# Kernel tuning notes

Measured on AMD Instinct MI355X. Metric: run time of the kernel, lower is better.

## Reference

```python
import jax, jax.numpy as jnp
import numpy as np

D = 2048      # hidden_size
S = 2048      # seq_len (batch packed, batch=1)
H = 16        # num_attention_heads
QL = 1536     # q_lora_rank
KVL = 512     # kv_lora_rank (latent dim, also v head size)
DN = 128      # qk_nope_head_dim
DR = 64       # qk_rope_head_dim
DV = 128      # v_head_dim
I = 8192      # mlp intermediate
EPS = 1e-6
SCALE = (DN + DR) ** -0.5  # softmax_scale = q_head_dim**-0.5 (no yarn mscale)


def rmsnorm(x, w):
    return x * jax.lax.rsqrt(jnp.mean(x * x, axis=-1, keepdims=True) + EPS) * w


def rotate_half(x):
    h = x.shape[-1] // 2
    return jnp.concatenate([-x[..., h:], x[..., :h]], axis=-1)


def setup_inputs() -> dict:
    key = jax.random.key(0)
    ks = jax.random.split(key, 10)
    s = 0.02
    # real RoPE tables (rotate_half layout)
    inv_freq = 1.0 / (10000.0 ** (jnp.arange(0, DR, 2, dtype=jnp.float32) / DR))
    t = jnp.arange(S, dtype=jnp.float32)
    emb = jnp.concatenate([jnp.outer(t, inv_freq)] * 2, axis=-1)  # [S, DR]
    return {
        'hidden_states': jax.random.normal(ks[0], (1, S, D), dtype=jnp.float32),
        'cos': jnp.cos(emb),
        'sin': jnp.sin(emb),
        'ln1_w': jnp.ones((D,), jnp.float32),
        'q_a_w': jax.random.normal(ks[1], (D, QL)) * s,
        'q_a_ln_w': jnp.ones((QL,), jnp.float32),
        'q_b_w': jax.random.normal(ks[2], (QL, H * (DN + DR))) * s,
        'kv_a_w': jax.random.normal(ks[3], (D, KVL + DR)) * s,
        'kv_a_ln_w': jnp.ones((KVL,), jnp.float32),
        'kc_w': jax.random.normal(ks[4], (H, DN, KVL)) * s,
        'vc_w': jax.random.normal(ks[5], (H, KVL, DV)) * s,
        'o_w': jax.random.normal(ks[6], (H * DV, D)) * s,
        'ln2_w': jnp.ones((D,), jnp.float32),
        'gate_up_w': jax.random.normal(ks[7], (D, 2 * I)) * s,
        'down_w': jax.random.normal(ks[8], (I, D)) * s,
    }


def reference(hidden_states, cos, sin, ln1_w, q_a_w, q_a_ln_w, q_b_w,
              kv_a_w, kv_a_ln_w, kc_w, vc_w, o_w, ln2_w, gate_up_w, down_w):
    residual = hidden_states
    h = rmsnorm(hidden_states, ln1_w)[0]                      # [S, D]
    # --- Q path: low-rank down + RMSNorm + up, split nope/rope ---
    q = rmsnorm(h @ q_a_w, q_a_ln_w) @ q_b_w                  # [S, H*(DN+DR)]
    q = q.reshape(S, H, DN + DR)
    q_nope, q_pe = q[..., :DN], q[..., DN:]
    # kc BMM: absorb W_UK, project q_nope into latent dim     # [S, H, KVL]
    q_lat = jnp.einsum('shd,hdc->shc', q_nope, kc_w)
    # --- KV path: compressed latent + shared rope key ---
    kv = h @ kv_a_w                                           # [S, KVL+DR]
    k_lat = rmsnorm(kv[:, :KVL], kv_a_ln_w)                   # [S, KVL] (also V)
    k_pe = kv[:, KVL:]                                        # [S, DR]
    # --- RoPE on the rope split only ---
    q_pe = q_pe * cos[:, None, :] + rotate_half(q_pe) * sin[:, None, :]
    k_pe = k_pe * cos + rotate_half(k_pe) * sin
    # --- latent MQA attention: q/k dim = KVL+DR, v dim = KVL ---
    qf = jnp.concatenate([q_lat, q_pe], axis=-1)              # [S, H, KVL+DR]
    kf = jnp.concatenate([k_lat, k_pe], axis=-1)              # [S, KVL+DR]
    scores = jnp.einsum('shc,tc->hst', qf, kf) * SCALE        # [H, S, S]
    causal = jnp.tril(jnp.ones((S, S), dtype=bool))
    scores = jnp.where(causal, scores, jnp.float32(-1e30))
    attn = jax.nn.softmax(scores, axis=-1)
    o_lat = jnp.einsum('hst,tc->shc', attn, k_lat)            # [S, H, KVL]
    # vc BMM: latent -> v_head_dim
    o = jnp.einsum('shc,hcv->shv', o_lat, vc_w).reshape(S, H * DV)
    attn_out = (o @ o_w)[None]                                # [1, S, D]
    hidden = residual + attn_out
    # --- dense SwiGLU MLP ---
    x2 = rmsnorm(hidden, ln2_w)
    gu = x2 @ gate_up_w
    mlp = (jax.nn.silu(gu[..., :I]) * gu[..., I:]) @ down_w
    return hidden + mlp
```

## Files before the change

kernel.cpp:

```cpp
#include <hip/hip_runtime.h>
#include <stdint.h>


#define S_   2048
#define D_   2048
#define H_   16
#define QL_  1536
#define KVL_ 512
#define DN_  128
#define DR_  64
#define DV_  128
#define I_   8192
#define SCALE_ 0.07216878364870323f

typedef __bf16 bf16x8 __attribute__((ext_vector_type(8)));
typedef float f32x4 __attribute__((ext_vector_type(4)));

__device__ __forceinline__ unsigned short f2bf(float f) {
  unsigned int u = __builtin_bit_cast(unsigned int, f);
  u += 0x7fffu + ((u >> 16) & 1u);
  return (unsigned short)(u >> 16);
}
__device__ __forceinline__ float bf2f(unsigned short b) {
  unsigned int u = ((unsigned int)b) << 16;
  return __builtin_bit_cast(float, u);
}

__device__ __forceinline__ float block_sum256(float v) {
  __shared__ float red[4];
  #pragma unroll
  for (int o = 32; o; o >>= 1) v += __shfl_xor(v, o);
  __syncthreads();
  if ((threadIdx.x & 63) == 0) red[threadIdx.x >> 6] = v;
  __syncthreads();
  return red[0] + red[1] + red[2] + red[3];
}
__device__ __forceinline__ float block_max256(float v) {
  __shared__ float red[4];
  #pragma unroll
  for (int o = 32; o; o >>= 1) v = fmaxf(v, __shfl_xor(v, o));
  __syncthreads();
  if ((threadIdx.x & 63) == 0) red[threadIdx.x >> 6] = v;
  __syncthreads();
  return fmaxf(fmaxf(red[0], red[1]), fmaxf(red[2], red[3]));
}

__device__ __forceinline__ void gload_lds16(const void* g, void* l) {
  void* gn = const_cast<void*>(g);
  __builtin_amdgcn_global_load_lds(
      (__attribute__((address_space(1))) void*)gn,
      (__attribute__((address_space(3))) void*)l, 16, 0, 0);
}

template <int OUT, int ADD_RES, int TRI, int CK>
__global__ __launch_bounds__(256) void gemm_bt(
    const unsigned short* __restrict__ A, const unsigned short* __restrict__ Bt,
    void* __restrict__ C, const float* __restrict__ R, float scale,
    int M, int N, int K, int lda, int ldb, int ldc,
    long sA, long sB, long sC) {
  __shared__ unsigned short As[128 * 64];
  __shared__ unsigned short Bs[128 * 64];
  const int b = blockIdx.z;
  int bx = blockIdx.x, by = blockIdx.y;
  if (TRI) {
    const int t = blockIdx.x;
    int i = (int)((sqrtf(8.f * t + 1.f) - 1.f) * 0.5f);
    while ((i + 1) * (i + 2) / 2 <= t) ++i;
    while (i * (i + 1) / 2 > t) --i;
    by = i;
    bx = t - i * (i + 1) / 2;
  }
  const int m0 = by * 128, n0 = bx * 128;
  if (CK) K = min(K, m0 + 128);
  const int tid = threadIdx.x, w = tid >> 6, lane = tid & 63;
  const int wm = (w >> 1) * 64, wn = (w & 1) * 64;
  const int fr = lane & 15;
  const int fq = lane >> 4;
  const int sr = lane >> 3;
  const int sch = (lane & 7) ^ sr;
  const unsigned short* Ab = A + (long)b * sA;
  const unsigned short* Bb = Bt + (long)b * sB;
  long aOff[4], bOff[4];
  #pragma unroll
  for (int i = 0; i < 4; ++i) {
    const int row = w * 32 + i * 8 + sr;
    aOff[i] = (long)(m0 + row) * lda + sch * 8;
    bOff[i] = (long)(n0 + row) * ldb + sch * 8;
  }
  const int ca0 = fq ^ (fr & 7);
  const int ca1 = (4 + fq) ^ (fr & 7);

  f32x4 acc[4][4] = {};

  for (int k0 = 0; k0 < K; k0 += 64) {
    #pragma unroll
    for (int i = 0; i < 4; ++i) {
      gload_lds16(Ab + aOff[i] + k0, As + (w * 32 + i * 8) * 64);
      gload_lds16(Bb + bOff[i] + k0, Bs + (w * 32 + i * 8) * 64);
    }
    __syncthreads();
    #pragma unroll
    for (int s = 0; s < 2; ++s) {
      const int cc = s ? ca1 : ca0;
      bf16x8 af[4], bf[4];
      #pragma unroll
      for (int i = 0; i < 4; ++i)
        af[i] = *(const bf16x8*)(As + (wm + i * 16 + fr) * 64 + cc * 8);
      #pragma unroll
      for (int j = 0; j < 4; ++j)
        bf[j] = *(const bf16x8*)(Bs + (wn + j * 16 + fr) * 64 + cc * 8);
      #pragma unroll
      for (int i = 0; i < 4; ++i)
        #pragma unroll
        for (int j = 0; j < 4; ++j)
          acc[i][j] = __builtin_amdgcn_mfma_f32_16x16x32_bf16(af[i], bf[j],
                                                              acc[i][j], 0, 0, 0);
    }
    __syncthreads();
  }

  const long cb = (long)b * sC;
  #pragma unroll
  for (int i = 0; i < 4; ++i) {
    const int row0 = m0 + wm + i * 16 + fq * 4;
    #pragma unroll
    for (int j = 0; j < 4; ++j) {
      const int col = n0 + wn + j * 16 + fr;
      #pragma unroll
      for (int r = 0; r < 4; ++r) {
        float v = acc[i][j][r] * scale;
        if (OUT == 2) {
          const float o = __shfl_xor(v, 1);
          const float res = v / (1.f + __expf(-v)) * o;
          if (((fr & 1) == 0) && col < N)
            ((unsigned short*)C)[cb + (long)(row0 + r) * ldc + (col >> 1)] =
                f2bf(res);
        } else {
          if (col < N) {
            const long idx = cb + (long)(row0 + r) * ldc + col;
            float vv = v;
            if (ADD_RES) vv += R[idx];
            if (OUT == 1) ((unsigned short*)C)[idx] = f2bf(vv);
            else          ((float*)C)[idx] = vv;
          }
        }
      }
    }
  }
}

__global__ void transpose_f2b(const float* __restrict__ in,
                              unsigned short* __restrict__ out, int Rr, int Cc,
                              long sIn, long sOut) {
  const int b = blockIdx.z;
  in += (long)b * sIn;
  out += (long)b * sOut;
  __shared__ float t[32][33];
  const int c0 = blockIdx.x * 32, r0 = blockIdx.y * 32;
  const int tx = threadIdx.x, ty = threadIdx.y;
  #pragma unroll
  for (int i = 0; i < 4; ++i)
    t[ty + i * 8][tx] = in[(long)(r0 + ty + i * 8) * Cc + c0 + tx];
  __syncthreads();
  #pragma unroll
  for (int i = 0; i < 4; ++i)
    out[(long)(c0 + ty + i * 8) * Rr + r0 + tx] = f2bf(t[tx][ty + i * 8]);
}

__global__ void transpose_f2b_ilv(const float* __restrict__ in,
                                  unsigned short* __restrict__ out) {
  __shared__ float t[32][33];
  const int c0 = blockIdx.x * 32, r0 = blockIdx.y * 32;
  const int tx = threadIdx.x, ty = threadIdx.y;
  #pragma unroll
  for (int i = 0; i < 4; ++i)
    t[ty + i * 8][tx] = in[(long)(r0 + ty + i * 8) * (2 * I_) + c0 + tx];
  __syncthreads();
  #pragma unroll
  for (int i = 0; i < 4; ++i) {
    const int c = c0 + ty + i * 8;
    const int n = ((c & (I_ - 1)) << 1) | (c >> 13);
    out[(long)n * D_ + r0 + tx] = f2bf(t[tx][ty + i * 8]);
  }
}

__global__ void rmsnorm_k(const float* __restrict__ x, const float* __restrict__ w,
                          unsigned short* __restrict__ y, int C) {
  const int row = blockIdx.x, tid = threadIdx.x;
  const float* xr = x + (long)row * C;
  float ss = 0.f;
  for (int c = tid; c < C; c += 256) { float v = xr[c]; ss += v * v; }
  ss = block_sum256(ss);
  const float rms = rsqrtf(ss / C + 1e-6f);
  for (int c = tid; c < C; c += 256)
    y[(long)row * C + c] = f2bf(xr[c] * rms * w[c]);
}

__global__ void q_post(const float* __restrict__ q, const float* __restrict__ cs,
                       const float* __restrict__ sn, unsigned short* __restrict__ qnope,
                       unsigned short* __restrict__ qf) {
  const int s = blockIdx.x, tid = threadIdx.x;
  const float* qr = q + (long)s * 3072;
  for (int c = tid; c < 3072; c += 256) {
    const int h = c / 192, d = c % 192;
    if (d < 128) {
      qnope[(long)s * 2048 + h * 128 + d] = f2bf(qr[c]);
    } else {
      const int j = d - 128;
      const float x = qr[c];
      const float rot = (j < 32) ? -qr[h * 192 + 128 + j + 32]
                                 :  qr[h * 192 + 128 + j - 32];
      const float v = x * cs[s * 64 + j] + rot * sn[s * 64 + j];
      qf[(long)h * (S_ * 576) + (long)s * 576 + 512 + j] = f2bf(v);
    }
  }
}

__global__ void kv_post(const float* __restrict__ kv, const float* __restrict__ w,
                        const float* __restrict__ cs, const float* __restrict__ sn,
                        unsigned short* __restrict__ kf, unsigned short* __restrict__ klt) {
  const int s = blockIdx.x, tid = threadIdx.x;
  const float* kr = kv + (long)s * 576;
  float ss = 0.f;
  for (int c = tid; c < 512; c += 256) { float v = kr[c]; ss += v * v; }
  ss = block_sum256(ss);
  const float rms = rsqrtf(ss / 512.f + 1e-6f);
  for (int c = tid; c < 576; c += 256) {
    if (c < 512) {
      const float v = kr[c] * rms * w[c];
      const unsigned short bv = f2bf(v);
      kf[(long)s * 576 + c] = bv;
      klt[(long)c * S_ + s] = bv;
    } else {
      const int j = c - 512;
      const float x = kr[c];
      const float rot = (j < 32) ? -kr[512 + j + 32] : kr[512 + j - 32];
      kf[(long)s * 576 + c] = f2bf(x * cs[s * 64 + j] + rot * sn[s * 64 + j]);
    }
  }
}

__global__ void softmax_causal_ip(unsigned short* __restrict__ sc, long hstride) {
  const int row = blockIdx.x, tid = threadIdx.x;
  unsigned short* sr = sc + (long)blockIdx.z * hstride + (long)row * S_;
  const int n = row + 1;
  const int kmax = ((row >> 7) + 1) << 7;
  float mx = -1e30f;
  for (int c = tid; c < n; c += 256) mx = fmaxf(mx, bf2f(sr[c]));
  mx = block_max256(mx);
  float e[8];
  float sum = 0.f;
  #pragma unroll
  for (int k = 0; k < 8; ++k) {
    const int c = tid + k * 256;
    if (c < n) { e[k] = __expf(bf2f(sr[c]) - mx); sum += e[k]; }
  }
  sum = block_sum256(sum);
  const float inv = 1.f / sum;
  #pragma unroll
  for (int k = 0; k < 8; ++k) {
    const int c = tid + k * 256;
    if (c < n) sr[c] = f2bf(e[k] * inv);
    else if (c < kmax) sr[c] = 0;
  }
}

extern "C" void kernel_launch(void* const* d_in, const int* in_sizes, int n_in,
                              void* d_out, int out_size, void* d_ws, size_t ws_size,
                              hipStream_t stream) {
  const float* hs   = (const float*)d_in[0];
  const float* cs   = (const float*)d_in[1];
  const float* sn   = (const float*)d_in[2];
  const float* ln1  = (const float*)d_in[3];
  const float* qaw  = (const float*)d_in[4];
  const float* qaln = (const float*)d_in[5];
  const float* qbw  = (const float*)d_in[6];
  const float* kvaw = (const float*)d_in[7];
  const float* kvln = (const float*)d_in[8];
  const float* kcw  = (const float*)d_in[9];
  const float* vcw  = (const float*)d_in[10];
  const float* ow   = (const float*)d_in[11];
  const float* ln2  = (const float*)d_in[12];
  const float* guw  = (const float*)d_in[13];
  const float* dww  = (const float*)d_in[14];
  float* out = (float*)d_out;
  char* ws = (char*)d_ws;

  unsigned short* hbf   = (unsigned short*)(ws + 0);
  float*          qa    = (float*)(ws + 8388608);
  unsigned short* qan   = (unsigned short*)(ws + 20971520);
  float*          q     = (float*)(ws + 27262976);
  unsigned short* qnope = (unsigned short*)(ws + 52428800);
  unsigned short* sc    = (unsigned short*)(ws + 0);
  unsigned short* qf    = (unsigned short*)(ws + 67108864);
  float*          kv    = (float*)(ws + 104857600);
  unsigned short* kf    = (unsigned short*)(ws + 109576192);
  unsigned short* klt   = (unsigned short*)(ws + 111935488);
  unsigned short* wt2   = (unsigned short*)(ws + 114032640);
  unsigned short* wt    = (unsigned short*)(ws + 116129792);
  unsigned short* olat  = (unsigned short*)(ws + 116129792);
  unsigned short* obf   = (unsigned short*)(ws + 0);
  float*          hidden= (float*)(ws + 8388608);
  unsigned short* x2    = (unsigned short*)(ws + 25165824);
  unsigned short* mlp   = (unsigned short*)(ws + 33554432);

  const dim3 B256(256), Bt32(32, 8);

  rmsnorm_k<<<S_, B256, 0, stream>>>(hs, ln1, hbf, D_);
  transpose_f2b<<<dim3(QL_/32, D_/32, 1), Bt32, 0, stream>>>(qaw, wt, D_, QL_, 0, 0);
  gemm_bt<0,0,0,0><<<dim3(QL_/128, S_/128, 1), B256, 0, stream>>>(
      hbf, wt, qa, nullptr, 1.f, S_, QL_, D_, D_, D_, QL_, 0, 0, 0);
  rmsnorm_k<<<S_, B256, 0, stream>>>(qa, qaln, qan, QL_);
  transpose_f2b<<<dim3(3072/32, QL_/32, 1), Bt32, 0, stream>>>(qbw, wt, QL_, 3072, 0, 0);
  gemm_bt<0,0,0,0><<<dim3(3072/128, S_/128, 1), B256, 0, stream>>>(
      qan, wt, q, nullptr, 1.f, S_, 3072, QL_, QL_, QL_, 3072, 0, 0, 0);
  q_post<<<S_, B256, 0, stream>>>(q, cs, sn, qnope, qf);
  transpose_f2b<<<dim3(576/32, D_/32, 1), Bt32, 0, stream>>>(kvaw, wt, D_, 576, 0, 0);
  gemm_bt<0,0,0,0><<<dim3(5, S_/128, 1), B256, 0, stream>>>(
      hbf, wt, kv, nullptr, 1.f, S_, 576, D_, D_, D_, 576, 0, 0, 0);
  kv_post<<<S_, B256, 0, stream>>>(kv, kvln, cs, sn, kf, klt);
  transpose_f2b<<<dim3(512/32, 128/32, H_), Bt32, 0, stream>>>(kcw, wt, 128, 512, 65536, 65536);
  transpose_f2b<<<dim3(128/32, 512/32, H_), Bt32, 0, stream>>>(vcw, wt2, 512, 128, 65536, 65536);
  gemm_bt<1,0,0,0><<<dim3(4, S_/128, H_), B256, 0, stream>>>(
      qnope, wt, qf, nullptr, 1.f, S_, 512, 128, 2048, 128, 576,
      128, 65536, (long)S_ * 576);
  for (int g = 0; g < 2; ++g) {
    const unsigned short* qfg = qf + (long)g * 8 * S_ * 576;
    gemm_bt<1,0,1,0><<<dim3(136, 1, 8), B256, 0, stream>>>(
        qfg, kf, sc, nullptr, SCALE_, S_, S_, 576, 576, 576, S_,
        (long)S_ * 576, 0, (long)S_ * S_);
    softmax_causal_ip<<<dim3(S_, 1, 8), B256, 0, stream>>>(sc, (long)S_ * S_);
    gemm_bt<1,0,0,1><<<dim3(4, 16, 8), B256, 0, stream>>>(
        sc, klt, olat + (long)g * 8 * S_ * 512, nullptr, 1.f,
        S_, 512, S_, S_, S_, 512, (long)S_ * S_, 0, (long)S_ * 512);
  }
  gemm_bt<1,0,0,0><<<dim3(1, S_/128, H_), B256, 0, stream>>>(
      olat, wt2, obf, nullptr, 1.f, S_, 128, 512, 512, 512, 2048,
      (long)S_ * 512, 65536, 128);
  transpose_f2b<<<dim3(D_/32, D_/32, 1), Bt32, 0, stream>>>(ow, wt, D_, D_, 0, 0);
  gemm_bt<0,1,0,0><<<dim3(D_/128, S_/128, 1), B256, 0, stream>>>(
      obf, wt, hidden, hs, 1.f, S_, D_, D_, D_, D_, D_, 0, 0, 0);
  rmsnorm_k<<<S_, B256, 0, stream>>>(hidden, ln2, x2, D_);
  transpose_f2b_ilv<<<dim3(2 * I_ / 32, D_/32, 1), Bt32, 0, stream>>>(guw, wt);
  gemm_bt<2,0,0,0><<<dim3(2 * I_ / 128, S_/128, 1), B256, 0, stream>>>(
      x2, wt, mlp, nullptr, 1.f, S_, 2 * I_, D_, D_, D_, I_, 0, 0, 0);
  transpose_f2b<<<dim3(D_/32, I_/32, 1), Bt32, 0, stream>>>(dww, wt, I_, D_, 0, 0);
  gemm_bt<0,1,0,0><<<dim3(D_/128, S_/128, 1), B256, 0, stream>>>(
      mlp, wt, out, hidden, 1.f, S_, D_, I_, I_, I_, D_, 0, 0, 0);
}
```

Baseline: 1.105 ms.

## Add 256x256 four-stage MFMA GEMM for scores and gate-up, widen transposes

Adds a new 512-thread GEMM kernel with 256x256 output tiles, a four-buffer LDS ring prefetching two K-steps ahead, XOR-swizzled LDS layout, an XCD-aware block remap, and split MFMA phases with priority hints. It is used for the causal QK^T score GEMM and the gate-up SwiGLU GEMM. The weight transpose kernels are replaced by a 64x64 tile version with float4 loads and 16-byte bf16 stores, with the interleave folded in as a template flag. The larger tiles aim to raise arithmetic intensity and cut global traffic, but use more registers and LDS, lowering occupancy. Edge handling for the 576-wide K and the triangular diagonal tiles rests on exact divisibility.

Result: no change. 1.119 ms (+1.2%).

```diff
diff --git a/kernel.cpp b/kernel.cpp
--- a/kernel.cpp
+++ b/kernel.cpp
@@ -15,6 +15,7 @@
 
 typedef __bf16 bf16x8 __attribute__((ext_vector_type(8)));
 typedef float f32x4 __attribute__((ext_vector_type(4)));
+typedef unsigned short us8 __attribute__((ext_vector_type(8)));
 
 __device__ __forceinline__ unsigned short f2bf(float f) {
   unsigned int u = __builtin_bit_cast(unsigned int, f);
@@ -50,6 +51,150 @@
   __builtin_amdgcn_global_load_lds(
       (__attribute__((address_space(1))) void*)gn,
       (__attribute__((address_space(3))) void*)l, 16, 0, 0);
+}
+
+template <int OUT, int TRI>
+__global__ __launch_bounds__(512, 2) void gemm256(
+    const unsigned short* __restrict__ A, const unsigned short* __restrict__ Bt,
+    void* __restrict__ C, float scale, int M, int N, int K,
+    int lda, int ldb, int ldc, long sA, long sB, long sC) {
+  __shared__ unsigned short As[4][8192];
+  __shared__ unsigned short Bs[4][8192];
+  const int b = blockIdx.z;
+  int bx = blockIdx.x, by = blockIdx.y;
+  if (TRI) {
+    const int t = blockIdx.x;
+    int i = (int)((sqrtf(8.f * t + 1.f) - 1.f) * 0.5f);
+    while ((i + 1) * (i + 2) / 2 <= t) ++i;
+    while (i * (i + 1) / 2 > t) --i;
+    by = i; bx = t - i * (i + 1) / 2;
+  } else {
+    int l = by * gridDim.x + bx;
+    const int nwg = gridDim.x * gridDim.y;
+    const int q = nwg >> 3, r = nwg & 7;
+    const int xcd = l & 7, pos = l >> 3;
+    l = (xcd < r ? xcd * (q + 1) : r * (q + 1) + (xcd - r) * q) + pos;
+    bx = l % gridDim.x; by = l / gridDim.x;
+  }
+  const int m0 = by * 256, n0 = bx * 256;
+  const int tid = threadIdx.x, w = tid >> 6, lane = tid & 63;
+  const int wm = w >> 2, wn = w & 3;
+  const int fr = lane & 15, fq = lane >> 4;
+  const unsigned short* Ab = A + (long)b * sA;
+  const unsigned short* Bb = Bt + (long)b * sB;
+
+  long aoff[2], boff[2];
+  int loff[2];
+  #pragma unroll
+  for (int j = 0; j < 2; ++j) {
+    const int g = (w + 8 * j) * 64 + lane;
+    const int row = g >> 2, c = g & 3;
+    const int sc_ = c ^ ((row >> 1) & 3);
+    aoff[j] = (long)(m0 + row) * lda + sc_ * 8;
+    boff[j] = (long)(n0 + row) * ldb + sc_ * 8;
+    loff[j] = g * 8;
+  }
+  const int NT = K >> 5;
+
+  #pragma unroll
+  for (int t = 0; t < 2; ++t) {
+    #pragma unroll
+    for (int j = 0; j < 2; ++j)
+      gload_lds16(Ab + aoff[j] + t * 32, As[t] + loff[j]);
+    #pragma unroll
+    for (int j = 0; j < 2; ++j)
+      gload_lds16(Bb + boff[j] + t * 32, Bs[t] + loff[j]);
+  }
+  asm volatile("s_waitcnt vmcnt(4)" ::: "memory");
+  asm volatile("s_barrier" ::: "memory");
+  __builtin_amdgcn_sched_barrier(0);
+
+  f32x4 acc[8][4] = {};
+  const int arow0 = wm * 128 + fr;
+  const int brow0 = wn * 64 + fr;
+
+  for (int kt = 0; kt < NT; ++kt) {
+    const unsigned short* At = As[kt & 3];
+    const unsigned short* Bl = Bs[kt & 3];
+    const bool pf = (kt + 2 < NT);
+    bf16x8 afrag[4], bfrag[4];
+    if (pf) {
+      #pragma unroll
+      for (int j = 0; j < 2; ++j)
+        gload_lds16(Ab + aoff[j] + (kt + 2) * 32, As[(kt + 2) & 3] + loff[j]);
+    }
+    #pragma unroll
+    for (int j = 0; j < 4; ++j) {
+      const int row = brow0 + j * 16;
+      bfrag[j] = *(const bf16x8*)(Bl + row * 32 + (fq ^ ((row >> 1) & 3)) * 8);
+    }
+    #pragma unroll
+    for (int i = 0; i < 4; ++i) {
+      const int row = arow0 + i * 16;
+      afrag[i] = *(const bf16x8*)(At + row * 32 + (fq ^ ((row >> 1) & 3)) * 8);
+    }
+    asm volatile("s_barrier" ::: "memory");
+    __builtin_amdgcn_sched_barrier(0);
+    __builtin_amdgcn_s_setprio(1);
+    #pragma unroll
+    for (int i = 0; i < 4; ++i)
+      #pragma unroll
+      for (int j = 0; j < 4; ++j)
+        acc[i][j] = __builtin_amdgcn_mfma_f32_16x16x32_bf16(
+            afrag[i], bfrag[j], acc[i][j], 0, 0, 0);
+    __builtin_amdgcn_s_setprio(0);
+    __builtin_amdgcn_sched_barrier(0);
+    if (pf) {
+      #pragma unroll
+      for (int j = 0; j < 2; ++j)
+        gload_lds16(Bb + boff[j] + (kt + 2) * 32, Bs[(kt + 2) & 3] + loff[j]);
+    }
+    #pragma unroll
+    for (int i = 0; i < 4; ++i) {
+      const int row = arow0 + 64 + i * 16;
+      afrag[i] = *(const bf16x8*)(At + row * 32 + (fq ^ ((row >> 1) & 3)) * 8);
+    }
+    if (kt + 1 < NT) {
+      if (pf) asm volatile("s_waitcnt vmcnt(4)" ::: "memory");
+      else    asm volatile("s_waitcnt vmcnt(0)" ::: "memory");
+      asm volatile("s_barrier" ::: "memory");
+      __builtin_amdgcn_sched_barrier(0);
+    }
+    __builtin_amdgcn_s_setprio(1);
+    #pragma unroll
+    for (int i = 0; i < 4; ++i)
+      #pragma unroll
+      for (int j = 0; j < 4; ++j)
+        acc[4 + i][j] = __builtin_amdgcn_mfma_f32_16x16x32_bf16(
+            afrag[i], bfrag[j], acc[4 + i][j], 0, 0, 0);
+    __builtin_amdgcn_s_setprio(0);
+    __builtin_amdgcn_sched_barrier(0);
+  }
+
+  const long cb = (long)b * sC;
+  #pragma unroll
+  for (int ii = 0; ii < 8; ++ii) {
+    const int row0 = m0 + wm * 128 + ii * 16 + fq * 4;
+    #pragma unroll
+    for (int j = 0; j < 4; ++j) {
+      const int col = n0 + wn * 64 + j * 16 + fr;
+      #pragma unroll
+      for (int r = 0; r < 4; ++r) {
+        float v = acc[ii][j][r] * scale;
+        if (OUT == 2) {
+          const float o = __shfl_xor(v, 1);
+          const float res = v / (1.f + __expf(-v)) * o;
+          if ((fr & 1) == 0)
+            ((unsigned short*)C)[cb + (long)(row0 + r) * ldc + (col >> 1)] =
+                f2bf(res);
+        } else if (OUT == 1) {
+          ((unsigned short*)C)[cb + (long)(row0 + r) * ldc + col] = f2bf(v);
+        } else {
+          ((float*)C)[cb + (long)(row0 + r) * ldc + col] = v;
+        }
+      }
+    }
+  }
 }
 
 template <int OUT, int ADD_RES, int TRI, int CK>
@@ -149,38 +294,38 @@
   }
 }
 
-__global__ void transpose_f2b(const float* __restrict__ in,
-                              unsigned short* __restrict__ out, int Rr, int Cc,
-                              long sIn, long sOut) {
+template <int ILV>
+__global__ __launch_bounds__(256) void transpose64(
+    const float* __restrict__ in, unsigned short* __restrict__ out,
+    int Rr, int Cc, long sIn, long sOut) {
+  __shared__ float t[64][65];
   const int b = blockIdx.z;
-  in += (long)b * sIn;
+  in  += (long)b * sIn;
   out += (long)b * sOut;
-  __shared__ float t[32][33];
-  const int c0 = blockIdx.x * 32, r0 = blockIdx.y * 32;
-  const int tx = threadIdx.x, ty = threadIdx.y;
-  #pragma unroll
-  for (int i = 0; i < 4; ++i)
-    t[ty + i * 8][tx] = in[(long)(r0 + ty + i * 8) * Cc + c0 + tx];
+  const int c0 = blockIdx.x * 64, r0 = blockIdx.y * 64;
+  const int tid = threadIdx.x;
+  const int rl = tid >> 4;
+  const int cq = tid & 15;
+  #pragma unroll
+  for (int rr = 0; rr < 4; ++rr) {
+    const int r = rl + rr * 16;
+    const float4 v = *(const float4*)(in + (long)(r0 + r) * Cc + c0 + cq * 4);
+    t[cq * 4 + 0][r] = v.x;
+    t[cq * 4 + 1][r] = v.y;
+    t[cq * 4 + 2][r] = v.z;
+    t[cq * 4 + 3][r] = v.w;
+  }
   __syncthreads();
-  #pragma unroll
-  for (int i = 0; i < 4; ++i)
-    out[(long)(c0 + ty + i * 8) * Rr + r0 + tx] = f2bf(t[tx][ty + i * 8]);
-}
-
-__global__ void transpose_f2b_ilv(const float* __restrict__ in,
-                                  unsigned short* __restrict__ out) {
-  __shared__ float t[32][33];
-  const int c0 = blockIdx.x * 32, r0 = blockIdx.y * 32;
-  const int tx = threadIdx.x, ty = threadIdx.y;
-  #pragma unroll
-  for (int i = 0; i < 4; ++i)
-    t[ty + i * 8][tx] = in[(long)(r0 + ty + i * 8) * (2 * I_) + c0 + tx];
-  __syncthreads();
-  #pragma unroll
-  for (int i = 0; i < 4; ++i) {
-    const int c = c0 + ty + i * 8;
-    const int n = ((c & (I_ - 1)) << 1) | (c >> 13);
-    out[(long)n * D_ + r0 + tx] = f2bf(t[tx][ty + i * 8]);
+  const int c = tid >> 2;
+  const int rb = (tid & 3) * 16;
+  const int cg = c0 + c;
+  const long nrow = ILV ? (long)(((cg & (I_ - 1)) << 1) | (cg >> 13)) : (long)cg;
+  #pragma unroll
+  for (int i = 0; i < 2; ++i) {
+    us8 o;
+    #pragma unroll
+    for (int jj = 0; jj < 8; ++jj) o[jj] = f2bf(t[c][rb + i * 8 + jj]);
+    *(us8*)(out + nrow * Rr + r0 + rb + i * 8) = o;
   }
 }
 
@@ -304,30 +449,30 @@
   unsigned short* x2    = (unsigned short*)(ws + 25165824);
   unsigned short* mlp   = (unsigned short*)(ws + 33554432);
 
-  const dim3 B256(256), Bt32(32, 8);
+  const dim3 B256(256), B512(512);
 
   rmsnorm_k<<<S_, B256, 0, stream>>>(hs, ln1, hbf, D_);
-  transpose_f2b<<<dim3(QL_/32, D_/32, 1), Bt32, 0, stream>>>(qaw, wt, D_, QL_, 0, 0);
+  transpose64<0><<<dim3(QL_/64, D_/64, 1), B256, 0, stream>>>(qaw, wt, D_, QL_, 0, 0);
   gemm_bt<0,0,0,0><<<dim3(QL_/128, S_/128, 1), B256, 0, stream>>>(
       hbf, wt, qa, nullptr, 1.f, S_, QL_, D_, D_, D_, QL_, 0, 0, 0);
   rmsnorm_k<<<S_, B256, 0, stream>>>(qa, qaln, qan, QL_);
-  transpose_f2b<<<dim3(3072/32, QL_/32, 1), Bt32, 0, stream>>>(qbw, wt, QL_, 3072, 0, 0);
+  transpose64<0><<<dim3(3072/64, QL_/64, 1), B256, 0, stream>>>(qbw, wt, QL_, 3072, 0, 0);
   gemm_bt<0,0,0,0><<<dim3(3072/128, S_/128, 1), B256, 0, stream>>>(
       qan, wt, q, nullptr, 1.f, S_, 3072, QL_, QL_, QL_, 3072, 0, 0, 0);
   q_post<<<S_, B256, 0, stream>>>(q, cs, sn, qnope, qf);
-  transpose_f2b<<<dim3(576/32, D_/32, 1), Bt32, 0, stream>>>(kvaw, wt, D_, 576, 0, 0);
+  transpose64<0><<<dim3(576/64, D_/64, 1), B256, 0, stream>>>(kvaw, wt, D_, 576, 0, 0);
   gemm_bt<0,0,0,0><<<dim3(5, S_/128, 1), B256, 0, stream>>>(
       hbf, wt, kv, nullptr, 1.f, S_, 576, D_, D_, D_, 576, 0, 0, 0);
   kv_post<<<S_, B256, 0, stream>>>(kv, kvln, cs, sn, kf, klt);
-  transpose_f2b<<<dim3(512/32, 128/32, H_), Bt32, 0, stream>>>(kcw, wt, 128, 512, 65536, 65536);
-  transpose_f2b<<<dim3(128/32, 512/32, H_), Bt32, 0, stream>>>(vcw, wt2, 512, 128, 65536, 65536);
+  transpose64<0><<<dim3(512/64, 128/64, H_), B256, 0, stream>>>(kcw, wt, 128, 512, 65536, 65536);
+  transpose64<0><<<dim3(128/64, 512/64, H_), B256, 0, stream>>>(vcw, wt2, 512, 128, 65536, 65536);
   gemm_bt<1,0,0,0><<<dim3(4, S_/128, H_), B256, 0, stream>>>(
       qnope, wt, qf, nullptr, 1.f, S_, 512, 128, 2048, 128, 576,
       128, 65536, (long)S_ * 576);
   for (int g = 0; g < 2; ++g) {
     const unsigned short* qfg = qf + (long)g * 8 * S_ * 576;
-    gemm_bt<1,0,1,0><<<dim3(136, 1, 8), B256, 0, stream>>>(
-        qfg, kf, sc, nullptr, SCALE_, S_, S_, 576, 576, 576, S_,
+    gemm256<1,1><<<dim3(36, 1, 8), B512, 0, stream>>>(
+        qfg, kf, sc, SCALE_, S_, S_, 576, 576, 576, S_,
         (long)S_ * 576, 0, (long)S_ * S_);
     softmax_causal_ip<<<dim3(S_, 1, 8), B256, 0, stream>>>(sc, (long)S_ * S_);
     gemm_bt<1,0,0,1><<<dim3(4, 16, 8), B256, 0, stream>>>(
@@ -337,14 +482,14 @@
   gemm_bt<1,0,0,0><<<dim3(1, S_/128, H_), B256, 0, stream>>>(
       olat, wt2, obf, nullptr, 1.f, S_, 128, 512, 512, 512, 2048,
       (long)S_ * 512, 65536, 128);
-  transpose_f2b<<<dim3(D_/32, D_/32, 1), Bt32, 0, stream>>>(ow, wt, D_, D_, 0, 0);
+  transpose64<0><<<dim3(D_/64, D_/64, 1), B256, 0, stream>>>(ow, wt, D_, D_, 0, 0);
   gemm_bt<0,1,0,0><<<dim3(D_/128, S_/128, 1), B256, 0, stream>>>(
       obf, wt, hidden, hs, 1.f, S_, D_, D_, D_, D_, D_, 0, 0, 0);
   rmsnorm_k<<<S_, B256, 0, stream>>>(hidden, ln2, x2, D_);
-  transpose_f2b_ilv<<<dim3(2 * I_ / 32, D_/32, 1), Bt32, 0, stream>>>(guw, wt);
-  gemm_bt<2,0,0,0><<<dim3(2 * I_ / 128, S_/128, 1), B256, 0, stream>>>(
-      x2, wt, mlp, nullptr, 1.f, S_, 2 * I_, D_, D_, D_, I_, 0, 0, 0);
-  transpose_f2b<<<dim3(D_/32, I_/32, 1), Bt32, 0, stream>>>(dww, wt, I_, D_, 0, 0);
+  transpose64<1><<<dim3(2 * I_ / 64, D_/64, 1), B256, 0, stream>>>(guw, wt, D_, 2 * I_, 0, 0);
+  gemm256<2,0><<<dim3(2 * I_ / 256, S_/256, 1), B512, 0, stream>>>(
+      x2, wt, mlp, 1.f, S_, 2 * I_, D_, D_, D_, I_, 0, 0, 0);
+  transpose64<0><<<dim3(D_/64, I_/64, 1), B256, 0, stream>>>(dww, wt, I_, D_, 0, 0);
   gemm_bt<0,1,0,0><<<dim3(D_/128, S_/128, 1), B256, 0, stream>>>(
       mlp, wt, out, hidden, 1.f, S_, D_, I_, I_, I_, D_, 0, 0, 0);
 }
```
